# Kernel optimization log

Measured on AMD Instinct MI355X. Metric: run time of the kernel, lower is better.

## Reference

```python
import jax, jax.numpy as jnp
import numpy as np

N = 100000
HEADS = 4
NHID = 32


def _gat_conv(x, src, dst, W, a_src, a_dst, b):
    # x: [N, Fin]; src/dst: [E'] (self-loops already appended)
    h = (x @ W).reshape(N, HEADS, NHID)                      # [N, H, D]
    al_src = jnp.einsum('nhd,hd->nh', h, a_src)              # [N, H]
    al_dst = jnp.einsum('nhd,hd->nh', h, a_dst)
    e = jax.nn.leaky_relu(al_src[src] + al_dst[dst], 0.2)    # [E', H]
    # segment softmax over incoming edges of each destination node
    m = jax.ops.segment_max(e, dst, num_segments=N)          # [N, H]
    ex = jnp.exp(e - m[dst])
    s = jax.ops.segment_sum(ex, dst, num_segments=N)         # [N, H]
    alpha = ex / (s[dst] + 1e-16)                            # [E', H]
    msg = h[src] * alpha[:, :, None]                         # [E', H, D]
    out = jax.ops.segment_sum(msg, dst, num_segments=N)      # [N, H, D]
    return out.reshape(N, HEADS * NHID) + b


def setup_inputs() -> dict:
    key = jax.random.key(0)
    ks = jax.random.split(key, 16)
    E = 1600000
    NFEAT, NCLASS = 128, 10
    width = HEADS * NHID  # 128
    sc = 0.1
    inp = {
        'x': jax.random.normal(ks[0], (N, NFEAT), jnp.float32),
        'edge_index': jax.random.randint(ks[1], (2, E), 0, N, jnp.int64)
            if jax.config.jax_enable_x64 else jax.random.randint(ks[1], (2, E), 0, N, jnp.int32),
        'W0': jax.random.normal(ks[2], (NFEAT, width), jnp.float32) * sc,
        'a_src0': jax.random.normal(ks[3], (HEADS, NHID), jnp.float32) * sc,
        'a_dst0': jax.random.normal(ks[4], (HEADS, NHID), jnp.float32) * sc,
        'b0': jnp.zeros((width,), jnp.float32),
        'W1': jax.random.normal(ks[5], (width, width), jnp.float32) * sc,
        'a_src1': jax.random.normal(ks[6], (HEADS, NHID), jnp.float32) * sc,
        'a_dst1': jax.random.normal(ks[7], (HEADS, NHID), jnp.float32) * sc,
        'b1': jnp.zeros((width,), jnp.float32),
        'W2': jax.random.normal(ks[8], (width, width), jnp.float32) * sc,
        'a_src2': jax.random.normal(ks[9], (HEADS, NHID), jnp.float32) * sc,
        'a_dst2': jax.random.normal(ks[10], (HEADS, NHID), jnp.float32) * sc,
        'b2': jnp.zeros((width,), jnp.float32),
        'fc_W': jax.random.normal(ks[11], (width, NCLASS), jnp.float32) * sc,
        'fc_b': jnp.zeros((NCLASS,), jnp.float32),
    }
    return inp


def reference(x, edge_index, W0, a_src0, a_dst0, b0, W1, a_src1, a_dst1, b1,
              W2, a_src2, a_dst2, b2, fc_W, fc_b):
    # PyG GATConv default add_self_loops=True
    loops = jnp.arange(N, dtype=edge_index.dtype)
    src = jnp.concatenate([edge_index[0], loops])
    dst = jnp.concatenate([edge_index[1], loops])
    h = x
    for (W, a_s, a_d, b) in ((W0, a_src0, a_dst0, b0),
                             (W1, a_src1, a_dst1, b1),
                             (W2, a_src2, a_dst2, b2)):
        h = jax.nn.elu(_gat_conv(h, src, dst, W, a_s, a_d, b))
        # F.dropout(training=False) -> identity
    logits = h @ fc_W + fc_b
    return jax.nn.log_softmax(logits, axis=1)
```

## Files before the change

kernel.cpp:

```cpp
#include <hip/hip_runtime.h>
#include <math.h>

#define NN 100000
#define FEAT 128
#define NHEAD 4
#define BSH 9
#define BNODES 512
#define NBUCK 196
#define BCAP 16384
#define PA_EPT 16
#define GTILES 6250
#define HSTRIDE 136
#define SRCMASK 0x1FFFF

typedef unsigned int uint;
typedef unsigned short ushort;
typedef __attribute__((ext_vector_type(8))) short short8;
typedef __attribute__((ext_vector_type(4))) float fx4;

__device__ __forceinline__ float lrelu(float v) { return v > 0.f ? v : 0.2f * v; }

__device__ __forceinline__ ushort f2bf(float f) {
    uint u = __float_as_uint(f);
    return (ushort)((u + 0x7fffu + ((u >> 16) & 1u)) >> 16);
}
__device__ __forceinline__ float bf_lo(uint u) { return __uint_as_float(u << 16); }
__device__ __forceinline__ float bf_hi(uint u) { return __uint_as_float(u & 0xffff0000u); }

__device__ __forceinline__ short8 pack8f(const float* p) {
    float4 a = *(const float4*)p, b = *(const float4*)(p + 4);
    short8 v;
    v[0] = (short)f2bf(a.x); v[1] = (short)f2bf(a.y);
    v[2] = (short)f2bf(a.z); v[3] = (short)f2bf(a.w);
    v[4] = (short)f2bf(b.x); v[5] = (short)f2bf(b.y);
    v[6] = (short)f2bf(b.z); v[7] = (short)f2bf(b.w);
    return v;
}

template <bool FP32IN>
__global__ __launch_bounds__(256, 2) void gemm_mfma_kernel(
    const void* __restrict__ in, const float* __restrict__ W,
    const float* __restrict__ a_src, const float* __restrict__ a_dst,
    ushort* __restrict__ hbf, float* __restrict__ al_s, float* __restrict__ al_d)
{
    __shared__ __align__(16) ushort WA[FEAT * FEAT];
    __shared__ __align__(16) ushort HS[4][16 * HSTRIDE];
    const int t = threadIdx.x;
    for (int idx = t; idx < FEAT * FEAT; idx += 256) {
        int k = idx >> 7, m = idx & 127;
        int mt = m >> 4, kt = k >> 5, qq = (k >> 3) & 3, j = k & 7;
        int ln = qq * 16 + (m & 15);
        WA[((mt * 4 + kt) * 64 + ln) * 8 + j] = f2bf(W[idx]);
    }
    __syncthreads();

    const int wv = t >> 6, lane = t & 63;
    const int node_l = lane & 15, q = lane >> 4;

    short8 afr[8][4];
    #pragma unroll
    for (int mt = 0; mt < 8; ++mt)
        #pragma unroll
        for (int kt = 0; kt < 4; ++kt)
            afr[mt][kt] = *(const short8*)&WA[((mt * 4 + kt) * 64 + lane) * 8];

    const ushort* inbf = (const ushort*)in;
    const float*  inf  = (const float*)in;

    for (int tile = blockIdx.x * 4 + wv; tile < GTILES; tile += gridDim.x * 4) {
        const int n0 = tile * 16;
        short8 b0, b1, b2, b3;
        if (FP32IN) {
            const float* rf = inf + (size_t)(n0 + node_l) * FEAT + q * 8;
            b0 = pack8f(rf);
            b1 = pack8f(rf + 32);
            b2 = pack8f(rf + 64);
            b3 = pack8f(rf + 96);
        } else {
            const ushort* rowp = inbf + (size_t)(n0 + node_l) * FEAT + q * 8;
            b0 = *(const short8*)(rowp);
            b1 = *(const short8*)(rowp + 32);
            b2 = *(const short8*)(rowp + 64);
            b3 = *(const short8*)(rowp + 96);
        }
        fx4 zero = {0.f, 0.f, 0.f, 0.f};
        fx4 acc[8];
        #pragma unroll
        for (int mt = 0; mt < 8; ++mt) acc[mt] = zero;
        #pragma unroll
        for (int kt = 0; kt < 4; ++kt) {
            short8 b = (kt == 0) ? b0 : (kt == 1) ? b1 : (kt == 2) ? b2 : b3;
            #pragma unroll
            for (int mt = 0; mt < 8; ++mt)
                acc[mt] = __builtin_amdgcn_mfma_f32_16x16x32_bf16(afr[mt][kt], b, acc[mt], 0, 0, 0);
        }
        float ps[4] = {0.f, 0.f, 0.f, 0.f};
        float pd[4] = {0.f, 0.f, 0.f, 0.f};
        #pragma unroll
        for (int mt = 0; mt < 8; ++mt) {
            float4 as4 = *(const float4*)(a_src + mt * 16 + q * 4);
            float4 ad4 = *(const float4*)(a_dst + mt * 16 + q * 4);
            ps[mt >> 1] += acc[mt][0] * as4.x + acc[mt][1] * as4.y + acc[mt][2] * as4.z + acc[mt][3] * as4.w;
            pd[mt >> 1] += acc[mt][0] * ad4.x + acc[mt][1] * ad4.y + acc[mt][2] * ad4.z + acc[mt][3] * ad4.w;
            ushort4 hv;
            hv.x = f2bf(acc[mt][0]); hv.y = f2bf(acc[mt][1]);
            hv.z = f2bf(acc[mt][2]); hv.w = f2bf(acc[mt][3]);
            *(ushort4*)&HS[wv][node_l * HSTRIDE + mt * 16 + q * 4] = hv;
        }
        #pragma unroll
        for (int h = 0; h < 4; ++h) {
            ps[h] += __shfl_xor(ps[h], 16); ps[h] += __shfl_xor(ps[h], 32);
            pd[h] += __shfl_xor(pd[h], 16); pd[h] += __shfl_xor(pd[h], 32);
        }
        float vs = (q == 0) ? ps[0] : (q == 1) ? ps[1] : (q == 2) ? ps[2] : ps[3];
        float vd = (q == 0) ? pd[0] : (q == 1) ? pd[1] : (q == 2) ? pd[2] : pd[3];
        al_s[(n0 + node_l) * 4 + q] = vs;
        al_d[(n0 + node_l) * 4 + q] = vd;
        #pragma unroll
        for (int it = 0; it < 4; ++it) {
            int fi = it * 64 + lane;
            int row = fi >> 4, colc = fi & 15;
            short8 v = *(const short8*)&HS[wv][row * HSTRIDE + colc * 8];
            *(short8*)(hbf + (size_t)n0 * FEAT + (size_t)fi * 8) = v;
        }
    }
}


__global__ void zero_small_kernel(int* bsize)
{
    int t = threadIdx.x;
    if (t < NBUCK) bsize[t] = 0;
}

__global__ __launch_bounds__(256) void bucket_hist_kernel(
    const int* __restrict__ ei, int E, int* bsize)
{
    __shared__ int lh[NBUCK];
    int t = threadIdx.x;
    if (t < NBUCK) lh[t] = 0;
    __syncthreads();
    int stride = gridDim.x * 256;
    for (int i = blockIdx.x * 256 + t; i < E + NN; i += stride) {
        int d = (i < E) ? ei[E + i] : (i - E);
        atomicAdd(&lh[d >> BSH], 1);
    }
    __syncthreads();
    if (t < NBUCK && lh[t]) atomicAdd(&bsize[t], lh[t]);
}

__global__ __launch_bounds__(256) void bucket_scan_kernel(
    const int* __restrict__ bsize, int* bbase, int* bcursor)
{
    __shared__ int sm[256];
    int t = threadIdx.x;
    int v = (t < NBUCK) ? bsize[t] : 0;
    sm[t] = v;
    __syncthreads();
    #pragma unroll
    for (int off = 1; off < 256; off <<= 1) {
        int x = (t >= off) ? sm[t - off] : 0;
        __syncthreads();
        sm[t] += x;
        __syncthreads();
    }
    if (t < NBUCK) {
        int excl = sm[t] - v;
        bbase[t] = excl;
        bcursor[t] = excl;
    }
    if (t == 255) bbase[NBUCK] = sm[255];
}

__global__ __launch_bounds__(256) void phaseA_bin_kernel(
    const int* __restrict__ ei, int E, int* bcursor, uint* __restrict__ pairs)
{
    __shared__ int lh[NBUCK], lb[NBUCK];
    int t = threadIdx.x;
    if (t < NBUCK) lh[t] = 0;
    __syncthreads();
    int base = blockIdx.x * (256 * PA_EPT) + t;
    int s[PA_EPT], d[PA_EPT];
    #pragma unroll
    for (int k = 0; k < PA_EPT; ++k) {
        int i = base + k * 256;
        if (i < E)            { s[k] = ei[i]; d[k] = ei[E + i]; }
        else if (i < E + NN)  { s[k] = i - E; d[k] = s[k]; }
        else                  { s[k] = 0; d[k] = -1; }
        if (d[k] >= 0) atomicAdd(&lh[d[k] >> BSH], 1);
    }
    __syncthreads();
    if (t < NBUCK) {
        int c = lh[t];
        lb[t] = c ? atomicAdd(&bcursor[t], c) : 0;
        lh[t] = 0;
    }
    __syncthreads();
    #pragma unroll
    for (int k = 0; k < PA_EPT; ++k) {
        if (d[k] >= 0) {
            int b = d[k] >> BSH;
            int off = atomicAdd(&lh[b], 1);
            pairs[lb[b] + off] = ((uint)(d[k] & (BNODES - 1)) << 17) | (uint)s[k];
        }
    }
}

__global__ __launch_bounds__(256) void phaseB_kernel(
    const uint* __restrict__ pairs, const int* __restrict__ bbase,
    int* __restrict__ row_ptr, int* __restrict__ colidx, int EP)
{
    __shared__ int nh[BNODES];
    __shared__ int ex[BNODES];
    __shared__ int ss[256];
    __shared__ int img[BCAP];
    int b = blockIdx.x, t = threadIdx.x;
    int node0 = b << BSH;
    int nend = min(NN - node0, BNODES);
    int pb = bbase[b], pe = bbase[b + 1];
    int span = pe - pb;
    for (int j = t; j < BNODES; j += 256) nh[j] = 0;
    __syncthreads();
    for (int i = t; i < span; i += 256)
        atomicAdd(&nh[pairs[pb + i] >> 17], 1);
    __syncthreads();
    int v0 = nh[2 * t], v1 = nh[2 * t + 1];
    int psc = v0 + v1;
    ss[t] = psc;
    __syncthreads();
    #pragma unroll
    for (int off = 1; off < 256; off <<= 1) {
        int x = (t >= off) ? ss[t - off] : 0;
        __syncthreads();
        ss[t] += x;
        __syncthreads();
    }
    int ep = ss[t] - psc;
    ex[2 * t] = ep;
    ex[2 * t + 1] = ep + v0;
    __syncthreads();
    for (int j = t; j < nend; j += 256) row_ptr[node0 + j] = pb + ex[j];
    if (b == NBUCK - 1 && t == 0) row_ptr[NN] = EP;
    for (int j = t; j < BNODES; j += 256) nh[j] = ex[j];
    __syncthreads();
    if (span <= BCAP) {
        for (int i = t; i < span; i += 256) {
            uint p = pairs[pb + i];
            int pos = atomicAdd(&nh[p >> 17], 1);
            img[pos] = (int)(p & SRCMASK);
        }
        __syncthreads();
        for (int i = t; i < span; i += 256) colidx[pb + i] = img[i];
    } else {
        for (int i = t; i < span; i += 256) {
            uint p = pairs[pb + i];
            int pos = atomicAdd(&nh[p >> 17], 1);
            colidx[pb + pos] = (int)(p & SRCMASK);
        }
    }
}

#define AGGR_STEP(hv, wgt)                                                    \
    a0 = fmaf(wgt, bf_lo(hv.x), a0); a1 = fmaf(wgt, bf_hi(hv.x), a1);        \
    a2 = fmaf(wgt, bf_lo(hv.y), a2); a3 = fmaf(wgt, bf_hi(hv.y), a3);        \
    a4 = fmaf(wgt, bf_lo(hv.z), a4); a5 = fmaf(wgt, bf_hi(hv.z), a5);        \
    a6 = fmaf(wgt, bf_lo(hv.w), a6); a7 = fmaf(wgt, bf_hi(hv.w), a7);

#define PROC4(cv)                                                             \
    {                                                                         \
        int s0 = cv.x, s1 = cv.y, s2 = cv.z, s3 = cv.w;                       \
        float w0 = __expf(lrelu(al_s[s0*4 + head] + ald_h));                  \
        float w1 = __expf(lrelu(al_s[s1*4 + head] + ald_h));                  \
        float w2 = __expf(lrelu(al_s[s2*4 + head] + ald_h));                  \
        float w3 = __expf(lrelu(al_s[s3*4 + head] + ald_h));                  \
        uint4 h0 = ((const uint4*)(hbf + (size_t)s0 * FEAT))[lane];           \
        uint4 h1 = ((const uint4*)(hbf + (size_t)s1 * FEAT))[lane];           \
        uint4 h2 = ((const uint4*)(hbf + (size_t)s2 * FEAT))[lane];           \
        uint4 h3 = ((const uint4*)(hbf + (size_t)s3 * FEAT))[lane];           \
        ssum += (w0 + w1) + (w2 + w3);                                        \
        AGGR_STEP(h0, w0) AGGR_STEP(h1, w1) AGGR_STEP(h2, w2) AGGR_STEP(h3, w3) \
    }

__global__ __launch_bounds__(256) void aggr_csr_kernel(
    const int* __restrict__ row_ptr, const int* __restrict__ colidx,
    const ushort* __restrict__ hbf, const float* __restrict__ al_s,
    const float* __restrict__ al_d, const float* __restrict__ bias,
    ushort* __restrict__ outbf)
{
    int t = threadIdx.x;
    int node = blockIdx.x * 16 + (t >> 4);
    if (node >= NN) return;
    int lane = t & 15;
    int head = lane >> 2;
    float ald_h = al_d[node * 4 + head];
    int beg = row_ptr[node], end = row_ptr[node + 1];

    float ssum = 0.f;
    float a0=0.f,a1=0.f,a2=0.f,a3=0.f,a4=0.f,a5=0.f,a6=0.f,a7=0.f;

    int p = beg;
    int4 ca;
    if (p + 4 <= end) ca = *(const int4*)&colidx[p];
    while (p + 8 <= end) {
        int4 na = *(const int4*)&colidx[p + 4];
        PROC4(ca)
        ca = na;
        p += 4;
    }
    if (p + 4 <= end) { PROC4(ca) p += 4; }
    for (; p < end; ++p) {
        int sn = colidx[p];
        float wq = __expf(lrelu(al_s[sn*4 + head] + ald_h));
        uint4 hv = ((const uint4*)(hbf + (size_t)sn * FEAT))[lane];
        ssum += wq;
        AGGR_STEP(hv, wq)
    }
    float inv = 1.f / (ssum + 1e-16f);
    const float* bp = bias + lane * 8;
    float o[8] = {a0,a1,a2,a3,a4,a5,a6,a7};
    #pragma unroll
    for (int k = 0; k < 8; ++k) {
        float v = o[k] * inv + bp[k];
        o[k] = v > 0.f ? v : __expf(v) - 1.f;
    }
    uint4 u;
    u.x = (uint)f2bf(o[0]) | ((uint)f2bf(o[1]) << 16);
    u.y = (uint)f2bf(o[2]) | ((uint)f2bf(o[3]) << 16);
    u.z = (uint)f2bf(o[4]) | ((uint)f2bf(o[5]) << 16);
    u.w = (uint)f2bf(o[6]) | ((uint)f2bf(o[7]) << 16);
    ((uint4*)(outbf + (size_t)node * FEAT))[lane] = u;
}

__global__ __launch_bounds__(256) void fc_kernel(
    const ushort* __restrict__ hbf, const float* __restrict__ fcW,
    const float* __restrict__ fcb, float* __restrict__ out)
{
    __shared__ float WT[10][FEAT];
    __shared__ float bl[10];
    int t = threadIdx.x;
    for (int i = t; i < FEAT * 10; i += 256) {
        int k = i / 10, c = i % 10;
        WT[c][k] = fcW[i];
    }
    if (t < 10) bl[t] = fcb[t];
    __syncthreads();
    int n = blockIdx.x * 256 + t;
    if (n >= NN) return;
    const uint4* row = (const uint4*)(hbf + (size_t)n * FEAT);
    float lg[10];
    #pragma unroll
    for (int c = 0; c < 10; ++c) lg[c] = bl[c];
    #pragma unroll 4
    for (int k8 = 0; k8 < 16; ++k8) {
        uint4 u = row[k8];
        float x0 = bf_lo(u.x), x1 = bf_hi(u.x), x2 = bf_lo(u.y), x3 = bf_hi(u.y);
        float x4 = bf_lo(u.z), x5 = bf_hi(u.z), x6 = bf_lo(u.w), x7 = bf_hi(u.w);
        #pragma unroll
        for (int c = 0; c < 10; ++c) {
            const float* wr = &WT[c][k8 * 8];
            float4 wa = *(const float4*)(wr);
            float4 wb = *(const float4*)(wr + 4);
            float acc = fmaf(x0, wa.x, fmaf(x1, wa.y, fmaf(x2, wa.z, x3 * wa.w)));
            acc = fmaf(x4, wb.x, fmaf(x5, wb.y, fmaf(x6, wb.z, fmaf(x7, wb.w, acc))));
            lg[c] += acc;
        }
    }
    float mx = lg[0];
    #pragma unroll
    for (int c = 1; c < 10; ++c) mx = fmaxf(mx, lg[c]);
    float se = 0.f;
    #pragma unroll
    for (int c = 0; c < 10; ++c) se += __expf(lg[c] - mx);
    float lse = mx + __logf(se);
    float2* op = (float2*)(out + (size_t)n * 10);
    #pragma unroll
    for (int c = 0; c < 5; ++c)
        op[c] = make_float2(lg[2*c] - lse, lg[2*c + 1] - lse);
}

extern "C" void kernel_launch(void* const* d_in, const int* in_sizes, int n_in,
                              void* d_out, int out_size, void* d_ws, size_t ws_size,
                              hipStream_t stream)
{
    const float* x   = (const float*)d_in[0];
    const int*   ei  = (const int*)d_in[1];
    const float* W[3]   = {(const float*)d_in[2], (const float*)d_in[6],  (const float*)d_in[10]};
    const float* asr[3] = {(const float*)d_in[3], (const float*)d_in[7],  (const float*)d_in[11]};
    const float* ads[3] = {(const float*)d_in[4], (const float*)d_in[8],  (const float*)d_in[12]};
    const float* bs[3]  = {(const float*)d_in[5], (const float*)d_in[9],  (const float*)d_in[13]};
    const float* fcW = (const float*)d_in[14];
    const float* fcb = (const float*)d_in[15];
    const int E  = in_sizes[1] / 2;
    const int EP = E + NN;

    ushort* hbf  = (ushort*)d_ws;
    ushort* ybf  = hbf + (size_t)NN * FEAT;
    float* als   = (float*)(ybf + (size_t)NN * FEAT);
    float* ald   = als + (size_t)NN * NHEAD;
    int* row_ptr = (int*)(ald + (size_t)NN * NHEAD);
    int* bsize   = row_ptr + NN + 1;
    int* bbase   = bsize + NBUCK;
    int* bcursor = bbase + NBUCK + 1;
    uint* pairs  = (uint*)(bcursor + NBUCK);
    int* colidx  = (int*)(pairs + (size_t)EP);

    zero_small_kernel<<<1, 256, 0, stream>>>(bsize);
    bucket_hist_kernel<<<1024, 256, 0, stream>>>(ei, E, bsize);
    bucket_scan_kernel<<<1, 256, 0, stream>>>(bsize, bbase, bcursor);
    phaseA_bin_kernel<<<(EP + 256*PA_EPT - 1) / (256*PA_EPT), 256, 0, stream>>>(ei, E, bcursor, pairs);
    phaseB_kernel<<<NBUCK, 256, 0, stream>>>(pairs, bbase, row_ptr, colidx, EP);

    gemm_mfma_kernel<true><<<512, 256, 0, stream>>>(x, W[0], asr[0], ads[0], hbf, als, ald);
    aggr_csr_kernel<<<(NN + 15) / 16, 256, 0, stream>>>(row_ptr, colidx, hbf, als, ald, bs[0], ybf);
    for (int l = 1; l < 3; ++l) {
        gemm_mfma_kernel<false><<<512, 256, 0, stream>>>(ybf, W[l], asr[l], ads[l], hbf, als, ald);
        aggr_csr_kernel<<<(NN + 15) / 16, 256, 0, stream>>>(row_ptr, colidx, hbf, als, ald, bs[l], ybf);
    }
    fc_kernel<<<(NN + 255) / 256, 256, 0, stream>>>(ybf, fcW, fcb, (float*)d_out);
}
```

Baseline: 493.7 us.

## Fuse final FC+log_softmax into last aggregation and co-schedule layer-0 GEMM with binning

The final classifier and log-softmax now run inside the last aggregation kernel. Each 16-lane group computes partial logits from its slice of the features, reduces them with shuffles, and writes the output directly, so the last bf16 activation write and re-read are gone. The layer-0 GEMM and the edge-binning phase A are merged into one launch with disjoint block ranges so the independent work can overlap, and a zeroing kernel becomes hipMemsetAsync. The trade-offs are a serial softmax on lane 0, extra shared memory in the aggregation kernel, and uneven block work in the combined launch.

```diff
diff --git a/kernel.cpp b/kernel.cpp
--- a/kernel.cpp
+++ b/kernel.cpp
@@ -10,6 +10,7 @@
 #define BCAP 16384
 #define PA_EPT 16
 #define GTILES 6250
+#define GEMMB 512
 #define HSTRIDE 136
 #define SRCMASK 0x1FFFF
 
@@ -38,10 +39,11 @@
 }
 
 template <bool FP32IN>
-__global__ __launch_bounds__(256, 2) void gemm_mfma_kernel(
+__device__ __forceinline__ void gemm_body(
     const void* __restrict__ in, const float* __restrict__ W,
     const float* __restrict__ a_src, const float* __restrict__ a_dst,
-    ushort* __restrict__ hbf, float* __restrict__ al_s, float* __restrict__ al_d)
+    ushort* __restrict__ hbf, float* __restrict__ al_s, float* __restrict__ al_d,
+    int bid, int gridn)
 {
     __shared__ __align__(16) ushort WA[FEAT * FEAT];
     __shared__ __align__(16) ushort HS[4][16 * HSTRIDE];
@@ -67,7 +69,7 @@
     const ushort* inbf = (const ushort*)in;
     const float*  inf  = (const float*)in;
 
-    for (int tile = blockIdx.x * 4 + wv; tile < GTILES; tile += gridDim.x * 4) {
+    for (int tile = bid * 4 + wv; tile < GTILES; tile += gridn * 4) {
         const int n0 = tile * 16;
         short8 b0, b1, b2, b3;
         if (FP32IN) {
@@ -126,60 +128,14 @@
     }
 }
 
-
-__global__ void zero_small_kernel(int* bsize)
-{
-    int t = threadIdx.x;
-    if (t < NBUCK) bsize[t] = 0;
-}
-
-__global__ __launch_bounds__(256) void bucket_hist_kernel(
-    const int* __restrict__ ei, int E, int* bsize)
-{
-    __shared__ int lh[NBUCK];
-    int t = threadIdx.x;
-    if (t < NBUCK) lh[t] = 0;
-    __syncthreads();
-    int stride = gridDim.x * 256;
-    for (int i = blockIdx.x * 256 + t; i < E + NN; i += stride) {
-        int d = (i < E) ? ei[E + i] : (i - E);
-        atomicAdd(&lh[d >> BSH], 1);
-    }
-    __syncthreads();
-    if (t < NBUCK && lh[t]) atomicAdd(&bsize[t], lh[t]);
-}
-
-__global__ __launch_bounds__(256) void bucket_scan_kernel(
-    const int* __restrict__ bsize, int* bbase, int* bcursor)
-{
-    __shared__ int sm[256];
-    int t = threadIdx.x;
-    int v = (t < NBUCK) ? bsize[t] : 0;
-    sm[t] = v;
-    __syncthreads();
-    #pragma unroll
-    for (int off = 1; off < 256; off <<= 1) {
-        int x = (t >= off) ? sm[t - off] : 0;
-        __syncthreads();
-        sm[t] += x;
-        __syncthreads();
-    }
-    if (t < NBUCK) {
-        int excl = sm[t] - v;
-        bbase[t] = excl;
-        bcursor[t] = excl;
-    }
-    if (t == 255) bbase[NBUCK] = sm[255];
-}
-
-__global__ __launch_bounds__(256) void phaseA_bin_kernel(
-    const int* __restrict__ ei, int E, int* bcursor, uint* __restrict__ pairs)
+__device__ __forceinline__ void phaseA_body(
+    const int* __restrict__ ei, int E, int* bcursor, uint* __restrict__ pairs, int bid)
 {
     __shared__ int lh[NBUCK], lb[NBUCK];
     int t = threadIdx.x;
     if (t < NBUCK) lh[t] = 0;
     __syncthreads();
-    int base = blockIdx.x * (256 * PA_EPT) + t;
+    int base = bid * (256 * PA_EPT) + t;
     int s[PA_EPT], d[PA_EPT];
     #pragma unroll
     for (int k = 0; k < PA_EPT; ++k) {
@@ -204,6 +160,66 @@
             pairs[lb[b] + off] = ((uint)(d[k] & (BNODES - 1)) << 17) | (uint)s[k];
         }
     }
+}
+
+__global__ __launch_bounds__(256, 2) void gemm_mfma_kernel(
+    const void* __restrict__ in, const float* __restrict__ W,
+    const float* __restrict__ a_src, const float* __restrict__ a_dst,
+    ushort* __restrict__ hbf, float* __restrict__ al_s, float* __restrict__ al_d)
+{
+    gemm_body<false>(in, W, a_src, a_dst, hbf, al_s, al_d, blockIdx.x, GEMMB);
+}
+
+__global__ __launch_bounds__(256, 2) void gemm0_phaseA_kernel(
+    const float* __restrict__ x, const float* __restrict__ W,
+    const float* __restrict__ a_src, const float* __restrict__ a_dst,
+    ushort* __restrict__ hbf, float* __restrict__ al_s, float* __restrict__ al_d,
+    const int* __restrict__ ei, int E, int* bcursor, uint* __restrict__ pairs)
+{
+    if (blockIdx.x < GEMMB)
+        gemm_body<true>(x, W, a_src, a_dst, hbf, al_s, al_d, blockIdx.x, GEMMB);
+    else
+        phaseA_body(ei, E, bcursor, pairs, blockIdx.x - GEMMB);
+}
+
+
+__global__ __launch_bounds__(256) void bucket_hist_kernel(
+    const int* __restrict__ ei, int E, int* bsize)
+{
+    __shared__ int lh[NBUCK];
+    int t = threadIdx.x;
+    if (t < NBUCK) lh[t] = 0;
+    __syncthreads();
+    int stride = gridDim.x * 256;
+    for (int i = blockIdx.x * 256 + t; i < E + NN; i += stride) {
+        int d = (i < E) ? ei[E + i] : (i - E);
+        atomicAdd(&lh[d >> BSH], 1);
+    }
+    __syncthreads();
+    if (t < NBUCK && lh[t]) atomicAdd(&bsize[t], lh[t]);
+}
+
+__global__ __launch_bounds__(256) void bucket_scan_kernel(
+    const int* __restrict__ bsize, int* bbase, int* bcursor)
+{
+    __shared__ int sm[256];
+    int t = threadIdx.x;
+    int v = (t < NBUCK) ? bsize[t] : 0;
+    sm[t] = v;
+    __syncthreads();
+    #pragma unroll
+    for (int off = 1; off < 256; off <<= 1) {
+        int x = (t >= off) ? sm[t - off] : 0;
+        __syncthreads();
+        sm[t] += x;
+        __syncthreads();
+    }
+    if (t < NBUCK) {
+        int excl = sm[t] - v;
+        bbase[t] = excl;
+        bcursor[t] = excl;
+    }
+    if (t == 255) bbase[NBUCK] = sm[255];
 }
 
 __global__ __launch_bounds__(256) void phaseB_kernel(
@@ -281,15 +297,27 @@
         AGGR_STEP(h0, w0) AGGR_STEP(h1, w1) AGGR_STEP(h2, w2) AGGR_STEP(h3, w3) \
     }
 
+template <bool LAST>
 __global__ __launch_bounds__(256) void aggr_csr_kernel(
     const int* __restrict__ row_ptr, const int* __restrict__ colidx,
     const ushort* __restrict__ hbf, const float* __restrict__ al_s,
     const float* __restrict__ al_d, const float* __restrict__ bias,
-    ushort* __restrict__ outbf)
-{
+    ushort* __restrict__ outbf,
+    const float* __restrict__ fcW, const float* __restrict__ fcb,
+    float* __restrict__ logout)
+{
+    __shared__ float WT[10][FEAT];
+    __shared__ float bl[10];
     int t = threadIdx.x;
+    if (LAST) {
+        for (int i = t; i < FEAT * 10; i += 256) {
+            int k = i / 10, c = i % 10;
+            WT[c][k] = fcW[i];
+        }
+        if (t < 10) bl[t] = fcb[t];
+        __syncthreads();
+    }
     int node = blockIdx.x * 16 + (t >> 4);
-    if (node >= NN) return;
     int lane = t & 15;
     int head = lane >> 2;
     float ald_h = al_d[node * 4 + head];
@@ -323,59 +351,45 @@
         float v = o[k] * inv + bp[k];
         o[k] = v > 0.f ? v : __expf(v) - 1.f;
     }
-    uint4 u;
-    u.x = (uint)f2bf(o[0]) | ((uint)f2bf(o[1]) << 16);
-    u.y = (uint)f2bf(o[2]) | ((uint)f2bf(o[3]) << 16);
-    u.z = (uint)f2bf(o[4]) | ((uint)f2bf(o[5]) << 16);
-    u.w = (uint)f2bf(o[6]) | ((uint)f2bf(o[7]) << 16);
-    ((uint4*)(outbf + (size_t)node * FEAT))[lane] = u;
-}
-
-__global__ __launch_bounds__(256) void fc_kernel(
-    const ushort* __restrict__ hbf, const float* __restrict__ fcW,
-    const float* __restrict__ fcb, float* __restrict__ out)
-{
-    __shared__ float WT[10][FEAT];
-    __shared__ float bl[10];
-    int t = threadIdx.x;
-    for (int i = t; i < FEAT * 10; i += 256) {
-        int k = i / 10, c = i % 10;
-        WT[c][k] = fcW[i];
-    }
-    if (t < 10) bl[t] = fcb[t];
-    __syncthreads();
-    int n = blockIdx.x * 256 + t;
-    if (n >= NN) return;
-    const uint4* row = (const uint4*)(hbf + (size_t)n * FEAT);
-    float lg[10];
-    #pragma unroll
-    for (int c = 0; c < 10; ++c) lg[c] = bl[c];
-    #pragma unroll 4
-    for (int k8 = 0; k8 < 16; ++k8) {
-        uint4 u = row[k8];
-        float x0 = bf_lo(u.x), x1 = bf_hi(u.x), x2 = bf_lo(u.y), x3 = bf_hi(u.y);
-        float x4 = bf_lo(u.z), x5 = bf_hi(u.z), x6 = bf_lo(u.w), x7 = bf_hi(u.w);
+    if (!LAST) {
+        uint4 u;
+        u.x = (uint)f2bf(o[0]) | ((uint)f2bf(o[1]) << 16);
+        u.y = (uint)f2bf(o[2]) | ((uint)f2bf(o[3]) << 16);
+        u.z = (uint)f2bf(o[4]) | ((uint)f2bf(o[5]) << 16);
+        u.w = (uint)f2bf(o[6]) | ((uint)f2bf(o[7]) << 16);
+        ((uint4*)(outbf + (size_t)node * FEAT))[lane] = u;
+    } else {
+        float lg[10];
         #pragma unroll
         for (int c = 0; c < 10; ++c) {
-            const float* wr = &WT[c][k8 * 8];
+            const float* wr = &WT[c][lane * 8];
             float4 wa = *(const float4*)(wr);
             float4 wb = *(const float4*)(wr + 4);
-            float acc = fmaf(x0, wa.x, fmaf(x1, wa.y, fmaf(x2, wa.z, x3 * wa.w)));
-            acc = fmaf(x4, wb.x, fmaf(x5, wb.y, fmaf(x6, wb.z, fmaf(x7, wb.w, acc))));
-            lg[c] += acc;
-        }
-    }
-    float mx = lg[0];
-    #pragma unroll
-    for (int c = 1; c < 10; ++c) mx = fmaxf(mx, lg[c]);
-    float se = 0.f;
-    #pragma unroll
-    for (int c = 0; c < 10; ++c) se += __expf(lg[c] - mx);
-    float lse = mx + __logf(se);
-    float2* op = (float2*)(out + (size_t)n * 10);
-    #pragma unroll
-    for (int c = 0; c < 5; ++c)
-        op[c] = make_float2(lg[2*c] - lse, lg[2*c + 1] - lse);
+            float acc = fmaf(o[0], wa.x, fmaf(o[1], wa.y, fmaf(o[2], wa.z, o[3] * wa.w)));
+            acc = fmaf(o[4], wb.x, fmaf(o[5], wb.y, fmaf(o[6], wb.z, fmaf(o[7], wb.w, acc))));
+            lg[c] = acc;
+        }
+        #pragma unroll
+        for (int c = 0; c < 10; ++c) {
+            lg[c] += __shfl_xor(lg[c], 1, 16);
+            lg[c] += __shfl_xor(lg[c], 2, 16);
+            lg[c] += __shfl_xor(lg[c], 4, 16);
+            lg[c] += __shfl_xor(lg[c], 8, 16);
+        }
+        if (lane == 0) {
+            float mx = -1e30f;
+            #pragma unroll
+            for (int c = 0; c < 10; ++c) { lg[c] += bl[c]; mx = fmaxf(mx, lg[c]); }
+            float se = 0.f;
+            #pragma unroll
+            for (int c = 0; c < 10; ++c) se += __expf(lg[c] - mx);
+            float lse = mx + __logf(se);
+            float2* op = (float2*)(logout + (size_t)node * 10);
+            #pragma unroll
+            for (int c = 0; c < 5; ++c)
+                op[c] = make_float2(lg[2*c] - lse, lg[2*c + 1] - lse);
+        }
+    }
 }
 
 extern "C" void kernel_launch(void* const* d_in, const int* in_sizes, int n_in,
@@ -404,17 +418,24 @@
     uint* pairs  = (uint*)(bcursor + NBUCK);
     int* colidx  = (int*)(pairs + (size_t)EP);
 
-    zero_small_kernel<<<1, 256, 0, stream>>>(bsize);
+    const int pab = (EP + 256 * PA_EPT - 1) / (256 * PA_EPT);
+
+    hipMemsetAsync(bsize, 0, NBUCK * sizeof(int), stream);
     bucket_hist_kernel<<<1024, 256, 0, stream>>>(ei, E, bsize);
     bucket_scan_kernel<<<1, 256, 0, stream>>>(bsize, bbase, bcursor);
-    phaseA_bin_kernel<<<(EP + 256*PA_EPT - 1) / (256*PA_EPT), 256, 0, stream>>>(ei, E, bcursor, pairs);
+
+    gemm0_phaseA_kernel<<<GEMMB + pab, 256, 0, stream>>>(
+        x, W[0], asr[0], ads[0], hbf, als, ald, ei, E, bcursor, pairs);
     phaseB_kernel<<<NBUCK, 256, 0, stream>>>(pairs, bbase, row_ptr, colidx, EP);
 
-    gemm_mfma_kernel<true><<<512, 256, 0, stream>>>(x, W[0], asr[0], ads[0], hbf, als, ald);
-    aggr_csr_kernel<<<(NN + 15) / 16, 256, 0, stream>>>(row_ptr, colidx, hbf, als, ald, bs[0], ybf);
-    for (int l = 1; l < 3; ++l) {
-        gemm_mfma_kernel<false><<<512, 256, 0, stream>>>(ybf, W[l], asr[l], ads[l], hbf, als, ald);
-        aggr_csr_kernel<<<(NN + 15) / 16, 256, 0, stream>>>(row_ptr, colidx, hbf, als, ald, bs[l], ybf);
-    }
-    fc_kernel<<<(NN + 255) / 256, 256, 0, stream>>>(ybf, fcW, fcb, (float*)d_out);
-}
+    aggr_csr_kernel<false><<<(NN + 15) / 16, 256, 0, stream>>>(
+        row_ptr, colidx, hbf, als, ald, bs[0], ybf, nullptr, nullptr, nullptr);
+
+    gemm_mfma_kernel<<<GEMMB, 256, 0, stream>>>(ybf, W[1], asr[1], ads[1], hbf, als, ald);
+    aggr_csr_kernel<false><<<(NN + 15) / 16, 256, 0, stream>>>(
+        row_ptr, colidx, hbf, als, ald, bs[1], ybf, nullptr, nullptr, nullptr);
+
+    gemm_mfma_kernel<<<GEMMB, 256, 0, stream>>>(ybf, W[2], asr[2], ads[2], hbf, als, ald);
+    aggr_csr_kernel<true><<<(NN + 15) / 16, 256, 0, stream>>>(
+        row_ptr, colidx, hbf, als, ald, bs[2], nullptr, fcW, fcb, (float*)d_out);
+}
```

New measurement: 479.4 us. 1.03x faster.
